# Performance work log

Hardware: AMD Instinct MI355X
Metric: run time of the kernel (lower is better)

The kernel has to match this reference:

```python
import jax, jax.numpy as jnp
import numpy as np

B, L, D = 1, 4096, 1024
H = 16
HD = D // H
SCALE = HD ** -0.5


def setup_inputs() -> dict:
    key = jax.random.key(0)
    k1, k2, k3 = jax.random.split(key, 3)
    X = jax.random.normal(k1, (B, L, D), dtype=jnp.float32)
    # torch Linear default init ~ U(-1/sqrt(fan_in), 1/sqrt(fan_in)); scaled normals are fine for a reference
    Wqkv = jax.random.normal(k2, (D, 3 * D), dtype=jnp.float32) * (D ** -0.5)
    bqkv = jnp.zeros((3 * D,), dtype=jnp.float32)
    Wproj = jax.random.normal(k3, (D, D), dtype=jnp.float32) * (D ** -0.5)
    bproj = jnp.zeros((D,), dtype=jnp.float32)
    return {"X": X, "Wqkv": Wqkv, "bqkv": bqkv, "Wproj": Wproj, "bproj": bproj}


def reference(X, Wqkv, bqkv, Wproj, bproj):
    Bn, Ln, Dn = X.shape
    qkv = X @ Wqkv + bqkv                       # [B, L, 3D]
    qkv = qkv.reshape(Bn, Ln, 3, H, HD)
    q, k, v = qkv[:, :, 0], qkv[:, :, 1], qkv[:, :, 2]   # [B, L, H, HD]
    # attention scores [B, H, L, L] (naive, matches original)
    attn = jnp.einsum('bqhd,bkhd->bhqk', q, k) * SCALE
    causal = jnp.tril(jnp.ones((Ln, Ln), dtype=bool))     # True = keep
    attn = jnp.where(causal, attn, -jnp.inf)
    score = jax.nn.softmax(attn, axis=-1)
    out = jnp.einsum('bhqk,bkhd->bqhd', score, v)         # [B, L, H, HD]
    out = out.reshape(Bn, Ln, Dn)
    return out @ Wproj + bproj
```

## Files before the change

kernel.cpp:

```cpp
#include <hip/hip_runtime.h>
#include <hip/hip_bf16.h>
#include <string.h>


typedef unsigned short ushort_t;
typedef __attribute__((ext_vector_type(8))) short short8;
typedef __attribute__((ext_vector_type(4))) short short4_t;
typedef __attribute__((ext_vector_type(4))) float f32x4;

#define MFMA16(a, b, c) __builtin_amdgcn_mfma_f32_16x16x32_bf16(a, b, c, 0, 0, 0)

#if __has_builtin(__builtin_amdgcn_mfma_f32_16x16x16bf16_1k)
#define HAVE_MFMA16K 1
__device__ __forceinline__ f32x4 mfma16x16(short4_t a, short4_t b, f32x4 c) {
    return __builtin_amdgcn_mfma_f32_16x16x16bf16_1k(a, b, c, 0, 0, 0);
}
#else
#define HAVE_MFMA16K 0
__device__ __forceinline__ f32x4 mfma16x16(short4_t a, short4_t b, f32x4 c) {
    asm("s_nop 1\n\tv_mfma_f32_16x16x16_bf16 %0, %1, %2, %0"
        : "+v"(c) : "v"(a), "v"(b));
    return c;
}
#endif

static constexpr int Lq = 4096;
static constexpr int Dm = 1024;
static constexpr int NH = 16;
static constexpr int HD = 64;
static constexpr int D3 = 3072;
static constexpr float SCALE_LOG2E = 0.125f * 1.44269504088896340736f;

__device__ __forceinline__ ushort_t f2bf(float f) {
    union { float f; unsigned int u; } x{f};
    unsigned int u = x.u;
    u += 0x7fffu + ((u >> 16) & 1u);
    return (ushort_t)(u >> 16);
}

__device__ __forceinline__ unsigned int cvtpk(float a, float b) {
    unsigned int r;
    asm("v_cvt_pk_bf16_f32 %0, %1, %2" : "=v"(r) : "v"(a), "v"(b));
    return r;
}

__device__ __forceinline__ void gl2lds16(const ushort_t* g, ushort_t* l) {
    __builtin_amdgcn_global_load_lds(
        (const __attribute__((address_space(1))) unsigned int*)g,
        (__attribute__((address_space(3))) unsigned int*)l, 16, 0, 0);
}

__global__ void __launch_bounds__(256)
prep(const float* __restrict__ X, const float* __restrict__ Wqkv,
     const float* __restrict__ Wproj, ushort_t* __restrict__ Xb,
     ushort_t* __restrict__ WqkvT, ushort_t* __restrict__ WprojT) {
    __shared__ float tile[32][33];
    const int bid = blockIdx.x, tid = threadIdx.x;
    if (bid < 4096) {
        int i = (bid * 256 + tid) * 4;
        float4 v = *(const float4*)&X[i];
        ushort_t r[4] = { f2bf(v.x), f2bf(v.y), f2bf(v.z), f2bf(v.w) };
        *(uint2*)&Xb[i] = *(uint2*)r;
        return;
    }
    const float* W; ushort_t* Wt; int Nd, nb, kb;
    if (bid < 7168) {
        int b = bid - 4096; W = Wqkv;  Wt = WqkvT;  Nd = 3072;
        nb = (b % 96) * 32; kb = (b / 96) * 32;
    } else {
        int b = bid - 7168; W = Wproj; Wt = WprojT; Nd = 1024;
        nb = (b % 32) * 32; kb = (b / 32) * 32;
    }
    const int tx = tid & 31, ty = tid >> 5;
    for (int j = 0; j < 32; j += 8)
        tile[ty + j][tx] = W[(size_t)(kb + ty + j) * Nd + nb + tx];
    __syncthreads();
    for (int j = 0; j < 32; j += 8)
        Wt[(size_t)(nb + ty + j) * Dm + kb + tx] = f2bf(tile[tx][ty + j]);
}

__global__ void __launch_bounds__(256)
gemm_qkv(const ushort_t* __restrict__ A, const ushort_t* __restrict__ Bt,
         const float* __restrict__ bias, ushort_t* __restrict__ Cq,
         ushort_t* __restrict__ Vt) {
    __shared__ alignas(16) ushort_t Alds[128 * 32];
    __shared__ alignas(16) ushort_t Blds[128 * 32];
    const int tid  = threadIdx.x;
    const int lane = tid & 63;
    const int w    = tid >> 6;
    const int quad = lane >> 4;
    const int l16  = lane & 15;
    const int mbase = blockIdx.x * 128;
    const int nbase = blockIdx.y * 128;
    const int moff  = (w >> 1) * 64;
    const int noff  = (w & 1) * 64;
    const int K = Dm;

    f32x4 acc[4][4] = {};

    for (int kb = 0; kb < K; kb += 32) {
        __syncthreads();
        #pragma unroll
        for (int c = 0; c < 2; c++) {
            int id  = w * 128 + c * 64 + lane;
            int row = id >> 2, col = (id & 3) * 8;
            gl2lds16(&A[(size_t)(mbase + row) * K + kb + col], &Alds[(size_t)(w * 128 + c * 64) * 8]);
            gl2lds16(&Bt[(size_t)(nbase + row) * K + kb + col], &Blds[(size_t)(w * 128 + c * 64) * 8]);
        }
        __syncthreads();
        short8 a[4], b[4];
        #pragma unroll
        for (int m = 0; m < 4; m++)
            a[m] = *(const short8*)&Alds[(moff + m * 16 + l16) * 32 + quad * 8];
        #pragma unroll
        for (int n = 0; n < 4; n++)
            b[n] = *(const short8*)&Blds[(noff + n * 16 + l16) * 32 + quad * 8];
        #pragma unroll
        for (int m = 0; m < 4; m++)
            #pragma unroll
            for (int n = 0; n < 4; n++)
                acc[m][n] = MFMA16(a[m], b[n], acc[m][n]);
    }

    if (nbase < 2048) {
        const bool qscale = (nbase < 1024);
        #pragma unroll
        for (int m = 0; m < 4; m++)
            #pragma unroll
            for (int n = 0; n < 4; n++)
                #pragma unroll
                for (int r = 0; r < 4; r++) {
                    int row = mbase + moff + m * 16 + quad * 4 + r;
                    int col = nbase + noff + n * 16 + l16;
                    float v = acc[m][n][r] + bias[col];
                    if (qscale) v *= SCALE_LOG2E;
                    Cq[(size_t)row * D3 + col] = f2bf(v);
                }
    } else {
        const int dbase = nbase - 2048 + noff;
        const size_t kb0 = (size_t)mbase + moff;
        #pragma unroll
        for (int n = 0; n < 4; n++) {
            const float bv = bias[nbase + noff + n * 16 + l16];
            ushort_t* vrow = Vt + (size_t)(dbase + n * 16 + l16) * Lq + kb0 + quad * 16;
            #pragma unroll
            for (int rp = 0; rp < 2; rp++) {
                ushort_t pk[8];
                #pragma unroll
                for (int dr = 0; dr < 2; dr++)
                    #pragma unroll
                    for (int m = 0; m < 4; m++)
                        pk[dr * 4 + m] = f2bf(acc[m][n][2 * rp + dr] + bv);
                *(short8*)(vrow + rp * 8) = *(const short8*)pk;
            }
        }
    }
}

__global__ void __launch_bounds__(1024)
attn_fwd(const ushort_t* __restrict__ qkv, const ushort_t* __restrict__ Vt,
         ushort_t* __restrict__ O) {
    union SMem {
        struct { ushort_t K[2][2][64 * 64]; ushort_t V[2][2][64 * 64]; } kv;
        float Ml[3 * 256 * 35];
    };
    __shared__ SMem sm;

    const int tid  = threadIdx.x;
    const int lane = tid & 63;
    const int w    = tid >> 6;
    const int qtr  = w >> 2;
    const int sub  = w & 3;
    const int quad = lane >> 4;
    const int l16  = lane & 15;
    const int bid  = blockIdx.x;
    const int h    = bid & 15;
    const int p    = bid >> 4;
    const float NEG_INF = -__builtin_inff();

    const ushort_t* kbase = qkv + Dm + h * HD;
    const ushort_t* vbase = Vt + (size_t)h * HD * Lq;

    int koff[2][2];
    #pragma unroll
    for (int s = 0; s < 2; s++) {
        const int tok = (l16 & 3) * 16 + (qtr & 1) * 8 + s * 4 + (l16 >> 2);
        const int fk  = ((l16 & 3) << 1) | ((l16 >> 2) & 1);
        #pragma unroll
        for (int kh = 0; kh < 2; kh++)
            koff[s][kh] = tok * 64 + (((kh * 4 + quad) ^ fk) * 8);
    }
    int voff[4][2];
    #pragma unroll
    for (int t4 = 0; t4 < 4; t4++)
        #pragma unroll
        for (int s = 0; s < 2; s++) {
            const int row = t4 * 16 + l16;
            const int g = (qtr & 1) * 4 + s * 2 + (quad >> 1);
            const int sx = (row & 7) ^ (((row >> 3) & 1) << 2);
            voff[t4][s] = row * 64 + ((g ^ sx) * 8) + (quad & 1) * 4;
        }
    const int kmc = (qtr >> 1) * 64 + (qtr & 1) * 8 + quad;

    const int  tv  = tid & 511;
    const int  rr  = tv >> 3;
    const int  ccK = (tv & 7) ^ ((((rr >> 4) & 3) << 1) | (rr & 1));
    const int  ccV = (tv & 7) ^ ((rr & 7) ^ (((rr >> 3) & 1) << 2));
    const bool isK = (tid < 512);
    const int  dsto = (w & 7) * 512;
    const ushort_t* kse = kbase + (size_t)rr * D3 + ccK * 8;
    const ushort_t* vse = vbase + (size_t)rr * Lq + ccV * 8;

    for (int sel = 0; sel < 2; sel++) {
        const int c      = sel ? (31 - p) : p;
        const int qc     = c * 128;
        const int rounds = c + 1;
        const int qrow0  = qc + sub * 32;

        short8 qf[2][2];
        #pragma unroll
        for (int m = 0; m < 2; m++) {
            const ushort_t* qr = qkv + (size_t)(qrow0 + m * 16 + l16) * D3 + h * HD;
            qf[m][0] = *(const short8*)(qr + quad * 8);
            qf[m][1] = *(const short8*)(qr + 32 + quad * 8);
        }

        f32x4 o[2][4] = {};
        float sacc[2] = { 0.f, 0.f };

        const ushort_t* kp = kse;
        const ushort_t* vp = vse;

        auto stage = [&](int b) {
            if (isK) {
                gl2lds16(kp,           &sm.kv.K[0][b][dsto]);
                gl2lds16(kp + 64 * D3, &sm.kv.K[1][b][dsto]);
            } else {
                gl2lds16(vp,           &sm.kv.V[0][b][dsto]);
                gl2lds16(vp + 64,      &sm.kv.V[1][b][dsto]);
            }
            kp += (size_t)128 * D3;
            vp += 128;
        };

        stage(0);

        for (int r = 0; r < rounds; r++) {
            const int buf = r & 1;
            __syncthreads();
            if (r + 1 < rounds) stage(buf ^ 1);

            const ushort_t* Kb = &sm.kv.K[qtr >> 1][buf][0];
            const ushort_t* Vb = &sm.kv.V[qtr >> 1][buf][0];
            const bool domask = (r == rounds - 1);

            short8 kf[2][2];
            #pragma unroll
            for (int s = 0; s < 2; s++)
                #pragma unroll
                for (int kh = 0; kh < 2; kh++)
                    kf[s][kh] = *(const short8*)&Kb[koff[s][kh]];
            short4_t vf[4][2];
            #pragma unroll
            for (int t4 = 0; t4 < 4; t4++)
                #pragma unroll
                for (int s = 0; s < 2; s++)
                    vf[t4][s] = *(const short4_t*)&Vb[voff[t4][s]];

            f32x4 st[2][2];
            __builtin_amdgcn_s_setprio(1);
            #pragma unroll
            for (int m = 0; m < 2; m++)
                #pragma unroll
                for (int s = 0; s < 2; s++) {
                    f32x4 t = {};
                    t = MFMA16(kf[s][0], qf[m][0], t);
                    t = MFMA16(kf[s][1], qf[m][1], t);
                    st[m][s] = t;
                }
            __builtin_amdgcn_s_setprio(0);

            short4_t pT[2][2];
            #pragma unroll
            for (int m = 0; m < 2; m++) {
                const int qg = qrow0 + m * 16 + l16;
                #pragma unroll
                for (int s = 0; s < 2; s++) {
                    float e[4];
                    #pragma unroll
                    for (int r4 = 0; r4 < 4; r4++) {
                        float v = st[m][s][r4];
                        if (domask && (r * 128 + kmc + s * 4 + r4 * 16 > qg))
                            v = NEG_INF;
                        e[r4] = __builtin_amdgcn_exp2f(v);
                    }
                    sacc[m] += (e[0] + e[1]) + (e[2] + e[3]);
                    union { unsigned int u[2]; short4_t s4; } pb;
                    pb.u[0] = cvtpk(e[0], e[1]);
                    pb.u[1] = cvtpk(e[2], e[3]);
                    pT[m][s] = pb.s4;
                }
            }

            __builtin_amdgcn_s_setprio(1);
            #pragma unroll
            for (int t4 = 0; t4 < 4; t4++)
                #pragma unroll
                for (int s = 0; s < 2; s++) {
                    o[0][t4] = mfma16x16(vf[t4][s], pT[0][s], o[0][t4]);
                    o[1][t4] = mfma16x16(vf[t4][s], pT[1][s], o[1][t4]);
                }
            __builtin_amdgcn_s_setprio(0);
        }

#if !HAVE_MFMA16K
        asm volatile("s_nop 7\n\ts_nop 7" ::: "memory");
#endif
        #pragma unroll
        for (int m = 0; m < 2; m++) {
            sacc[m] += __shfl_xor(sacc[m], 16);
            sacc[m] += __shfl_xor(sacc[m], 32);
        }

        __syncthreads();
        if (qtr != 0) {
            float* dst = sm.Ml + (size_t)((qtr - 1) * 256 + sub * 64 + lane) * 35;
            #pragma unroll
            for (int m = 0; m < 2; m++)
                #pragma unroll
                for (int t4 = 0; t4 < 4; t4++)
                    *(f32x4*)(dst + (m * 4 + t4) * 4) = o[m][t4];
            dst[32] = sacc[0];
            dst[33] = sacc[1];
        }
        __syncthreads();
        if (qtr == 0) {
            #pragma unroll
            for (int j = 0; j < 3; j++) {
                const float* src = sm.Ml + (size_t)(j * 256 + sub * 64 + lane) * 35;
                #pragma unroll
                for (int m = 0; m < 2; m++)
                    #pragma unroll
                    for (int t4 = 0; t4 < 4; t4++)
                        o[m][t4] += *(const f32x4*)(src + (m * 4 + t4) * 4);
                sacc[0] += src[32];
                sacc[1] += src[33];
            }
            #pragma unroll
            for (int m = 0; m < 2; m++) {
                const float inv = 1.0f / sacc[m];
                ushort_t* orow = O + (size_t)(qrow0 + m * 16 + l16) * Dm + h * HD;
                #pragma unroll
                for (int t4 = 0; t4 < 4; t4++) {
                    ushort_t pk[4];
                    #pragma unroll
                    for (int r4 = 0; r4 < 4; r4++)
                        pk[r4] = f2bf(o[m][t4][r4] * inv);
                    *(uint2*)(orow + t4 * 16 + quad * 4) = *(const uint2*)pk;
                }
            }
        }
        __syncthreads();
    }
}

__global__ void __launch_bounds__(256)
gemm_proj(const ushort_t* __restrict__ A, const ushort_t* __restrict__ Bt,
          const float* __restrict__ bias, float* __restrict__ C) {
    __shared__ alignas(16) ushort_t Alds[128 * 32];
    __shared__ alignas(16) ushort_t Blds[64 * 32];
    const int tid  = threadIdx.x;
    const int lane = tid & 63;
    const int w    = tid >> 6;
    const int quad = lane >> 4;
    const int l16  = lane & 15;
    const int mbase = blockIdx.x * 128;
    const int nbase = blockIdx.y * 64;
    const int moff  = (w >> 1) * 64;
    const int noff  = (w & 1) * 32;
    const int K = Dm, N = Dm;

    f32x4 acc[4][2] = {};

    for (int kb = 0; kb < K; kb += 32) {
        __syncthreads();
        #pragma unroll
        for (int c = 0; c < 2; c++) {
            int id  = w * 128 + c * 64 + lane;
            int row = id >> 2, col = (id & 3) * 8;
            gl2lds16(&A[(size_t)(mbase + row) * K + kb + col], &Alds[(size_t)(w * 128 + c * 64) * 8]);
        }
        {
            int id  = w * 64 + lane;
            int row = id >> 2, col = (id & 3) * 8;
            gl2lds16(&Bt[(size_t)(nbase + row) * K + kb + col], &Blds[(size_t)(w * 64) * 8]);
        }
        __syncthreads();
        short8 a[4], b[2];
        #pragma unroll
        for (int m = 0; m < 4; m++)
            a[m] = *(const short8*)&Alds[(moff + m * 16 + l16) * 32 + quad * 8];
        #pragma unroll
        for (int n = 0; n < 2; n++)
            b[n] = *(const short8*)&Blds[(noff + n * 16 + l16) * 32 + quad * 8];
        #pragma unroll
        for (int m = 0; m < 4; m++)
            #pragma unroll
            for (int n = 0; n < 2; n++)
                acc[m][n] = MFMA16(a[m], b[n], acc[m][n]);
    }

    #pragma unroll
    for (int m = 0; m < 4; m++)
        #pragma unroll
        for (int n = 0; n < 2; n++)
            #pragma unroll
            for (int r = 0; r < 4; r++) {
                int row = mbase + moff + m * 16 + quad * 4 + r;
                int col = nbase + noff + n * 16 + l16;
                C[(size_t)row * N + col] = acc[m][n][r] + bias[col];
            }
}

extern "C" void kernel_launch(void* const* d_in, const int* in_sizes, int n_in,
                              void* d_out, int out_size, void* d_ws, size_t ws_size,
                              hipStream_t stream) {
    const float* X     = (const float*)d_in[0];
    const float* Wqkv  = (const float*)d_in[1];
    const float* bqkv  = (const float*)d_in[2];
    const float* Wproj = (const float*)d_in[3];
    const float* bproj = (const float*)d_in[4];
    float* out = (float*)d_out;

    ushort_t* ws     = (ushort_t*)d_ws;
    ushort_t* Xb     = ws;
    ushort_t* WqkvT  = Xb + (size_t)Lq * Dm;
    ushort_t* WprojT = WqkvT + (size_t)D3 * Dm;
    ushort_t* qkvB   = WprojT + (size_t)Dm * Dm;
    ushort_t* VtB    = qkvB + (size_t)Lq * D3;
    ushort_t* Ob     = VtB + (size_t)NH * HD * Lq;

    prep<<<dim3(8192), 256, 0, stream>>>(X, Wqkv, Wproj, Xb, WqkvT, WprojT);

    gemm_qkv<<<dim3(Lq / 128, D3 / 128), 256, 0, stream>>>(
        Xb, WqkvT, bqkv, qkvB, VtB);

    attn_fwd<<<dim3(256), 1024, 0, stream>>>(qkvB, VtB, Ob);

    gemm_proj<<<dim3(Lq / 128, Dm / 64), 256, 0, stream>>>(
        Ob, WprojT, bproj, out);
}
```

Baseline: 205.6 us.

## Deepen GEMM K-step to 64, swizzle block order, add occupancy hints

```diff
diff --git a/kernel.cpp b/kernel.cpp
--- a/kernel.cpp
+++ b/kernel.cpp
@@ -79,47 +79,59 @@
         Wt[(size_t)(nb + ty + j) * Dm + kb + tx] = f2bf(tile[tx][ty + j]);
 }
 
-__global__ void __launch_bounds__(256)
+__global__ void __launch_bounds__(256, 3)
 gemm_qkv(const ushort_t* __restrict__ A, const ushort_t* __restrict__ Bt,
          const float* __restrict__ bias, ushort_t* __restrict__ Cq,
          ushort_t* __restrict__ Vt) {
-    __shared__ alignas(16) ushort_t Alds[128 * 32];
-    __shared__ alignas(16) ushort_t Blds[128 * 32];
+    __shared__ alignas(16) ushort_t Alds[2][128 * 32];
+    __shared__ alignas(16) ushort_t Blds[2][128 * 32];
     const int tid  = threadIdx.x;
     const int lane = tid & 63;
     const int w    = tid >> 6;
     const int quad = lane >> 4;
     const int l16  = lane & 15;
-    const int mbase = blockIdx.x * 128;
-    const int nbase = blockIdx.y * 128;
+    const int lin0 = blockIdx.y * 32 + blockIdx.x;
+    const int lin  = (lin0 & 7) * 96 + (lin0 >> 3);
+    const int mbase = (lin & 31) * 128;
+    const int nbase = (lin >> 5) * 128;
     const int moff  = (w >> 1) * 64;
     const int noff  = (w & 1) * 64;
     const int K = Dm;
 
     f32x4 acc[4][4] = {};
 
-    for (int kb = 0; kb < K; kb += 32) {
-        __syncthreads();
-        #pragma unroll
-        for (int c = 0; c < 2; c++) {
-            int id  = w * 128 + c * 64 + lane;
-            int row = id >> 2, col = (id & 3) * 8;
-            gl2lds16(&A[(size_t)(mbase + row) * K + kb + col], &Alds[(size_t)(w * 128 + c * 64) * 8]);
-            gl2lds16(&Bt[(size_t)(nbase + row) * K + kb + col], &Blds[(size_t)(w * 128 + c * 64) * 8]);
-        }
-        __syncthreads();
-        short8 a[4], b[4];
+    for (int kb = 0; kb < K; kb += 64) {
+        __syncthreads();
+        #pragma unroll
+        for (int c = 0; c < 4; c++) {
+            const int id    = c * 256 + w * 64 + lane;
+            const int plane = id >> 9;
+            const int rem   = id & 511;
+            const int row   = rem >> 2, col = (rem & 3) * 8;
+            ushort_t* dstA = &Alds[plane][(size_t)((c & 1) * 256 + w * 64) * 8];
+            ushort_t* dstB = &Blds[plane][(size_t)((c & 1) * 256 + w * 64) * 8];
+            gl2lds16(&A[(size_t)(mbase + row) * K + kb + plane * 32 + col], dstA);
+            gl2lds16(&Bt[(size_t)(nbase + row) * K + kb + plane * 32 + col], dstB);
+        }
+        __syncthreads();
+        short8 a[4][2], b[4][2];
         #pragma unroll
         for (int m = 0; m < 4; m++)
-            a[m] = *(const short8*)&Alds[(moff + m * 16 + l16) * 32 + quad * 8];
+            #pragma unroll
+            for (int kk = 0; kk < 2; kk++)
+                a[m][kk] = *(const short8*)&Alds[kk][(moff + m * 16 + l16) * 32 + quad * 8];
         #pragma unroll
         for (int n = 0; n < 4; n++)
-            b[n] = *(const short8*)&Blds[(noff + n * 16 + l16) * 32 + quad * 8];
-        #pragma unroll
-        for (int m = 0; m < 4; m++)
-            #pragma unroll
-            for (int n = 0; n < 4; n++)
-                acc[m][n] = MFMA16(a[m], b[n], acc[m][n]);
+            #pragma unroll
+            for (int kk = 0; kk < 2; kk++)
+                b[n][kk] = *(const short8*)&Blds[kk][(noff + n * 16 + l16) * 32 + quad * 8];
+        #pragma unroll
+        for (int kk = 0; kk < 2; kk++)
+            #pragma unroll
+            for (int m = 0; m < 4; m++)
+                #pragma unroll
+                for (int n = 0; n < 4; n++)
+                    acc[m][n] = MFMA16(a[m][kk], b[n][kk], acc[m][n]);
     }
 
     if (nbase < 2048) {
@@ -364,50 +376,65 @@
     }
 }
 
-__global__ void __launch_bounds__(256)
+__global__ void __launch_bounds__(256, 2)
 gemm_proj(const ushort_t* __restrict__ A, const ushort_t* __restrict__ Bt,
           const float* __restrict__ bias, float* __restrict__ C) {
-    __shared__ alignas(16) ushort_t Alds[128 * 32];
-    __shared__ alignas(16) ushort_t Blds[64 * 32];
+    __shared__ alignas(16) ushort_t Alds[2][128 * 32];
+    __shared__ alignas(16) ushort_t Blds[2][64 * 32];
     const int tid  = threadIdx.x;
     const int lane = tid & 63;
     const int w    = tid >> 6;
     const int quad = lane >> 4;
     const int l16  = lane & 15;
-    const int mbase = blockIdx.x * 128;
-    const int nbase = blockIdx.y * 64;
+    const int lin0 = blockIdx.y * 32 + blockIdx.x;
+    const int lin  = (lin0 & 7) * 64 + (lin0 >> 3);
+    const int mbase = (lin & 31) * 128;
+    const int nbase = (lin >> 5) * 64;
     const int moff  = (w >> 1) * 64;
     const int noff  = (w & 1) * 32;
     const int K = Dm, N = Dm;
 
     f32x4 acc[4][2] = {};
 
-    for (int kb = 0; kb < K; kb += 32) {
-        __syncthreads();
+    for (int kb = 0; kb < K; kb += 64) {
+        __syncthreads();
+        #pragma unroll
+        for (int c = 0; c < 4; c++) {
+            const int id    = c * 256 + w * 64 + lane;
+            const int plane = id >> 9;
+            const int rem   = id & 511;
+            const int row   = rem >> 2, col = (rem & 3) * 8;
+            gl2lds16(&A[(size_t)(mbase + row) * K + kb + plane * 32 + col],
+                     &Alds[plane][(size_t)((c & 1) * 256 + w * 64) * 8]);
+        }
         #pragma unroll
         for (int c = 0; c < 2; c++) {
-            int id  = w * 128 + c * 64 + lane;
-            int row = id >> 2, col = (id & 3) * 8;
-            gl2lds16(&A[(size_t)(mbase + row) * K + kb + col], &Alds[(size_t)(w * 128 + c * 64) * 8]);
-        }
-        {
-            int id  = w * 64 + lane;
-            int row = id >> 2, col = (id & 3) * 8;
-            gl2lds16(&Bt[(size_t)(nbase + row) * K + kb + col], &Blds[(size_t)(w * 64) * 8]);
-        }
-        __syncthreads();
-        short8 a[4], b[2];
+            const int id    = c * 256 + w * 64 + lane;
+            const int plane = id >> 8;
+            const int rem   = id & 255;
+            const int row   = rem >> 2, col = (rem & 3) * 8;
+            gl2lds16(&Bt[(size_t)(nbase + row) * K + kb + plane * 32 + col],
+                     &Blds[plane][(size_t)(w * 64) * 8]);
+        }
+        __syncthreads();
+        short8 a[4][2], b[2][2];
         #pragma unroll
         for (int m = 0; m < 4; m++)
-            a[m] = *(const short8*)&Alds[(moff + m * 16 + l16) * 32 + quad * 8];
+            #pragma unroll
+            for (int kk = 0; kk < 2; kk++)
+                a[m][kk] = *(const short8*)&Alds[kk][(moff + m * 16 + l16) * 32 + quad * 8];
         #pragma unroll
         for (int n = 0; n < 2; n++)
-            b[n] = *(const short8*)&Blds[(noff + n * 16 + l16) * 32 + quad * 8];
-        #pragma unroll
-        for (int m = 0; m < 4; m++)
-            #pragma unroll
-            for (int n = 0; n < 2; n++)
-                acc[m][n] = MFMA16(a[m], b[n], acc[m][n]);
+            #pragma unroll
+            for (int kk = 0; kk < 2; kk++)
+                b[n][kk] = *(const short8*)&Blds[kk][(noff + n * 16 + l16) * 32 + quad * 8];
+        #pragma unroll
+        for (int kk = 0; kk < 2; kk++)
+            #pragma unroll
+            for (int m = 0; m < 4; m++)
+                #pragma unroll
+                for (int n = 0; n < 2; n++)
+                    acc[m][n] = MFMA16(a[m][kk], b[n][kk], acc[m][n]);
     }
 
     #pragma unroll
```

Result: faster. 196.6 us (-4.4%).
